# Optimization experiments

Hardware: AMD Instinct MI355X
Metric: run time of the kernel (lower is better)

The kernel has to match this reference:

```python
import jax, jax.numpy as jnp
import numpy as np


def setup_inputs() -> dict:
    key = jax.random.key(0)
    k1, k2 = jax.random.split(key)
    x = jax.random.normal(k1, (8, 2048, 512), dtype=jnp.float32)
    codebook = jax.random.normal(k2, (8192, 512), dtype=jnp.float32)
    return {"x": x, "codebook": codebook}


def reference(x, codebook):
    # x: [B, S, D]; codebook: [K, D]
    B, S, D = x.shape
    flat_x = x.reshape(-1, D)  # [N, D], N = B*S
    # argmin over L2 distance == argmin over squared L2 distance:
    x_sq = jnp.sum(flat_x * flat_x, axis=-1, keepdims=True)        # [N, 1]
    c_sq = jnp.sum(codebook * codebook, axis=-1)                   # [K]
    dots = jnp.einsum('nd,kd->nk', flat_x, codebook)               # [N, K]
    dist_sq = x_sq - 2.0 * dots + c_sq[None, :]                    # [N, K]
    indices = jnp.argmin(dist_sq, axis=1)                          # [N]
    quantized = jnp.take(codebook, indices, axis=0)                # [N, D]
    return quantized.reshape(x.shape)
```

## Files before the change

### kernel.cpp

```cpp
#include <hip/hip_runtime.h>
#include <cstdint>

constexpr int DD = 512;
constexpr int KK = 8192;
constexpr int NROWS = 16384;
#define MARGIN 1.0f

constexpr size_t AX_ELEMS = (size_t)NROWS * DD;
constexpr size_t BF_ELEMS = (size_t)KK * DD;
constexpr size_t KEY_ELEMS = (size_t)NROWS * 128;
constexpr size_t WS_NEEDED =
    AX_ELEMS * 2 + BF_ELEMS * 2 + (size_t)KK * 4 + KEY_ELEMS * 8;

typedef __attribute__((ext_vector_type(8))) short short8v;
typedef __attribute__((ext_vector_type(8))) _Float16 half8v;
typedef __attribute__((ext_vector_type(4))) float floatx4;
typedef unsigned long long ull;

__device__ __forceinline__ ull umin64(ull a, ull b) { return a < b ? a : b; }
__device__ __forceinline__ uint32_t fsort(float f) {
  uint32_t u = __float_as_uint(f);
  return (u & 0x80000000u) ? ~u : (u | 0x80000000u);
}
__device__ __forceinline__ float funsort(uint32_t u) {
  uint32_t f = (u & 0x80000000u) ? (u ^ 0x80000000u) : ~u;
  return __uint_as_float(f);
}

__device__ __forceinline__ void gl_lds16(const ushort* g, ushort* l) {
  __builtin_amdgcn_global_load_lds(
      (const __attribute__((address_space(1))) unsigned int*)g,
      (__attribute__((address_space(3))) unsigned int*)l, 16, 0, 0);
}

__device__ __forceinline__ float pairwise128_sq(const float* __restrict__ p) {
#pragma clang fp contract(off)
  float r[8];
  {
    float4 a = ((const float4*)p)[0];
    float4 b = ((const float4*)p)[1];
    r[0] = a.x * a.x; r[1] = a.y * a.y; r[2] = a.z * a.z; r[3] = a.w * a.w;
    r[4] = b.x * b.x; r[5] = b.y * b.y; r[6] = b.z * b.z; r[7] = b.w * b.w;
  }
  for (int i = 2; i < 32; i += 2) {
    float4 a = ((const float4*)p)[i];
    float4 b = ((const float4*)p)[i + 1];
    r[0] = r[0] + a.x * a.x; r[1] = r[1] + a.y * a.y;
    r[2] = r[2] + a.z * a.z; r[3] = r[3] + a.w * a.w;
    r[4] = r[4] + b.x * b.x; r[5] = r[5] + b.y * b.y;
    r[6] = r[6] + b.z * b.z; r[7] = r[7] + b.w * b.w;
  }
  return ((r[0] + r[1]) + (r[2] + r[3])) + ((r[4] + r[5]) + (r[6] + r[7]));
}

__global__ __launch_bounds__(256)
void cast16_kernel(const float* __restrict__ src, ushort* __restrict__ dst) {
  int idx = blockIdx.x * 256 + threadIdx.x;
  float4 v = *(const float4*)(src + (size_t)idx * 4);
  ushort h[4];
  float vv[4] = {v.x, v.y, v.z, v.w};
#pragma unroll
  for (int i = 0; i < 4; ++i) h[i] = __builtin_bit_cast(ushort, (_Float16)vv[i]);
  *(ushort4*)(dst + (size_t)idx * 4) = make_ushort4(h[0], h[1], h[2], h[3]);
}

__global__ __launch_bounds__(256)
void csq_kernel(const float* __restrict__ CB, float* __restrict__ csq) {
  __shared__ float cblk[64][4];
  int t = threadIdx.x;
  int r0 = blockIdx.x * 64;
  int row = t >> 2, blk = t & 3;
  cblk[row][blk] = pairwise128_sq(CB + (size_t)(r0 + row) * DD + blk * 128);
  __syncthreads();
  if (t < 64) {
#pragma clang fp contract(off)
    csq[r0 + t] = (cblk[t][0] + cblk[t][1]) + (cblk[t][2] + cblk[t][3]);
  }
}

__global__ __launch_bounds__(256, 4)
void vq_screen16_kernel(const ushort* __restrict__ Axp, const ushort* __restrict__ Bfp,
                        const float* __restrict__ csq, ull* __restrict__ keys) {
  __shared__ ushort AS[128 * 64];
  __shared__ ushort BS[128 * 64];
  __shared__ ull mb[128][2][2];

  const int t = threadIdx.x;
  const int L = t & 63;
  const int w = t >> 6;
  const int wr = (w >> 1) * 64, wc = (w & 1) * 64;

  const int bid = blockIdx.x;
  const int swz = (bid & 7) * 1024 + (bid >> 3);
  const int rb = swz & 127, cb = swz >> 7;
  const size_t r0 = (size_t)rb * 128, c0 = (size_t)cb * 128;

  const int lrow = L >> 3;
  const int lgr = (L & 7) ^ lrow;
  const ushort* srcA0 = Axp + (r0 + w * 32 + lrow) * DD + lgr * 8;
  const ushort* srcB0 = Bfp + (c0 + w * 32 + lrow) * DD + lgr * 8;

  floatx4 acc[4][4];
#pragma unroll
  for (int m = 0; m < 4; ++m)
#pragma unroll
    for (int n = 0; n < 4; ++n) acc[m][n] = (floatx4){0.f, 0.f, 0.f, 0.f};

  for (int kc = 0; kc < 8; ++kc) {
    if (kc) __syncthreads();
#pragma unroll
    for (int j = 0; j < 4; ++j) {
      gl_lds16(srcA0 + (size_t)j * 8 * DD + kc * 64, &AS[(w * 32 + j * 8) * 64]);
      gl_lds16(srcB0 + (size_t)j * 8 * DD + kc * 64, &BS[(w * 32 + j * 8) * 64]);
    }
    __syncthreads();

#pragma unroll
    for (int s = 0; s < 2; ++s) {
      const int kcol = s * 4 + (L >> 4);
      half8v af[4], bf[4];
#pragma unroll
      for (int m = 0; m < 4; ++m) {
        const int rl = wr + m * 16 + (L & 15);
        af[m] = *(const half8v*)&AS[rl * 64 + ((kcol * 8) ^ ((rl & 7) * 8))];
      }
#pragma unroll
      for (int n = 0; n < 4; ++n) {
        const int cl = wc + n * 16 + (L & 15);
        bf[n] = *(const half8v*)&BS[cl * 64 + ((kcol * 8) ^ ((cl & 7) * 8))];
      }
#pragma unroll
      for (int m = 0; m < 4; ++m)
#pragma unroll
        for (int n = 0; n < 4; ++n)
          acc[m][n] = __builtin_amdgcn_mfma_f32_16x16x32_f16(af[m], bf[n], acc[m][n], 0, 0, 0);
    }
  }

  float cq[4];
#pragma unroll
  for (int n = 0; n < 4; ++n) cq[n] = csq[c0 + wc + n * 16 + (L & 15)];

#pragma unroll
  for (int m = 0; m < 4; ++m) {
#pragma unroll
    for (int i = 0; i < 4; ++i) {
      ull k1 = ~0ull, k2 = ~0ull;
#pragma unroll
      for (int n = 0; n < 4; ++n) {
        float q = cq[n] - 2.0f * acc[m][n][i];
        ull key = ((ull)fsort(q) << 32) | (uint32_t)(c0 + wc + n * 16 + (L & 15));
        if (key < k1) { k2 = k1; k1 = key; }
        else if (key < k2) k2 = key;
      }
#pragma unroll
      for (int mask = 1; mask <= 8; mask <<= 1) {
        ull o1 = __shfl_xor(k1, mask, 64);
        ull o2 = __shfl_xor(k2, mask, 64);
        if (o1 < k1) { ull n2 = umin64(k1, o2); k1 = o1; k2 = n2; }
        else { k2 = umin64(o1, k2); }
      }
      if ((L & 15) == 0) {
        int rl = wr + m * 16 + (L >> 4) * 4 + i;
        mb[rl][w & 1][0] = k1;
        mb[rl][w & 1][1] = k2;
      }
    }
  }
  __syncthreads();
  if (t < 128) {
    ull a1 = mb[t][0][0], a2 = mb[t][0][1];
    ull b1 = mb[t][1][0], b2 = mb[t][1][1];
    ull k1, k2;
    if (a1 < b1) { k1 = a1; k2 = umin64(a2, b1); }
    else { k1 = b1; k2 = umin64(b2, a1); }
    keys[(r0 + t) * 128 + cb * 2 + 0] = k1;
    keys[(r0 + t) * 128 + cb * 2 + 1] = k2;
  }
}

__global__ __launch_bounds__(256)
void vq_reduce_kernel(const float* __restrict__ X, const float* __restrict__ CB,
                      const float* __restrict__ csq, const ull* __restrict__ keys,
                      float* __restrict__ out) {
  __shared__ int bidx[4];
  const int t = threadIdx.x;
  const int L = t & 63;
  const int w = t >> 6;
  const size_t row = (size_t)blockIdx.x * 4 + w;
  ulonglong2 kk = *(const ulonglong2*)(keys + row * 128 + L * 2);

  ull kmin = umin64(kk.x, kk.y);
#pragma unroll
  for (int m = 32; m; m >>= 1) {
    ull o = __shfl_xor(kmin, m, 64);
    if (o < kmin) kmin = o;
  }
  const float qcut = funsort((uint32_t)(kmin >> 32)) + MARGIN;

  const bool q0 = funsort((uint32_t)(kk.x >> 32)) <= qcut;
  const bool q1 = funsort((uint32_t)(kk.y >> 32)) <= qcut;
  const ull b0 = __ballot(q0);
  const ull b1 = __ballot(q1);
  const int total = __popcll(b0) + __popcll(b1);

  int winner;
  if (total <= 1) {
    winner = (int)(kmin & 0xffffffffu);
  } else {
    const float* xp = X + row * DD;
    const float4 xa = ((const float4*)xp)[L * 2];
    const float4 xb = ((const float4*)xp)[L * 2 + 1];
    ull bestE = ~0ull;
#pragma unroll
    for (int pass = 0; pass < 2; ++pass) {
      ull mask = pass ? b1 : b0;
      while (mask) {
        const int lane = __ffsll(mask) - 1;
        mask &= mask - 1;
        const ull key = __shfl(pass ? kk.y : kk.x, lane, 64);
        const int idx = (int)(key & 0xffffffffu);
        const float* cp = CB + (size_t)idx * DD;
        const float4 ca = ((const float4*)cp)[L * 2];
        const float4 cbv = ((const float4*)cp)[L * 2 + 1];
        float p = 0.f;
        p = __builtin_fmaf(xa.x, ca.x, p);
        p = __builtin_fmaf(xa.y, ca.y, p);
        p = __builtin_fmaf(xa.z, ca.z, p);
        p = __builtin_fmaf(xa.w, ca.w, p);
        p = __builtin_fmaf(xb.x, cbv.x, p);
        p = __builtin_fmaf(xb.y, cbv.y, p);
        p = __builtin_fmaf(xb.z, cbv.z, p);
        p = __builtin_fmaf(xb.w, cbv.w, p);
#pragma unroll
        for (int m = 32; m; m >>= 1) p += __shfl_xor(p, m, 64);
        const float q = csq[idx] - 2.0f * p;
        const ull ek = ((ull)fsort(q) << 32) | (uint32_t)idx;
        bestE = umin64(bestE, ek);
      }
    }
    winner = (int)(bestE & 0xffffffffu);
  }
  if (L == 0) bidx[w] = winner;
  __syncthreads();

  const size_t r0 = (size_t)blockIdx.x * 4;
#pragma unroll
  for (int it = 0; it < 2; ++it) {
    int idx = t + it * 256;
    int rw = idx >> 7, c4 = idx & 127;
    float4 v = *(const float4*)(CB + (size_t)bidx[rw] * DD + c4 * 4);
    *(float4*)(out + (r0 + rw) * DD + c4 * 4) = v;
  }
}

constexpr int FBM = 128, FBN = 128, FBK = 32, FNT = 256;
constexpr int FKSPLIT = 4;
constexpr int FKPB = KK / FKSPLIT;

__global__ __launch_bounds__(FNT)
void vq_partial_kernel(const float* __restrict__ X, const float* __restrict__ CB,
                       float* __restrict__ keyout) {
  __shared__ float Xs[FBK][FBM + 4];
  __shared__ float Cs[FBK][FBN + 4];
  __shared__ float xblk[FBM][4];
  __shared__ float cblk[FBN][4];
  __shared__ float xsq[FBM];
  __shared__ float csq[FBN];

  const int t = threadIdx.x;
  const int tx = t & 15;
  const int ty = t >> 4;
  const int bid = blockIdx.x;
  const int xcd = bid & 7;
  const int loc = bid >> 3;
  const int ksplit = xcd >> 1;
  const int rowblk = (xcd & 1) * 64 + loc;
  const long r0 = (long)rowblk * FBM;
  const int kbase = ksplit * FKPB;

#pragma unroll
  for (int it = 0; it < 2; ++it) {
    int task = t + it * FNT;
    int row = task >> 2, blk = task & 3;
    xblk[row][blk] = pairwise128_sq(X + (r0 + row) * DD + blk * 128);
  }
  __syncthreads();
  if (t < FBM) {
#pragma clang fp contract(off)
    xsq[t] = (xblk[t][0] + xblk[t][1]) + (xblk[t][2] + xblk[t][3]);
  }

  uint64_t bestKey[8];
#pragma unroll
  for (int i = 0; i < 8; ++i) bestKey[i] = ~0ull;

  float4 xr[4], cr[4];
  for (int kt = 0; kt < FKPB / FBN; ++kt) {
    const int k0 = kbase + kt * FBN;
    __syncthreads();
#pragma unroll
    for (int it = 0; it < 4; ++it) {
      int idx = t + it * FNT;
      int row = idx >> 3, dg = (idx & 7) * 4;
      xr[it] = *(const float4*)(X + (r0 + row) * DD + dg);
      cr[it] = *(const float4*)(CB + (long)(k0 + row) * DD + dg);
    }
#pragma unroll
    for (int it = 0; it < 2; ++it) {
      int task = t + it * FNT;
      int cw = task >> 2, blk = task & 3;
      cblk[cw][blk] = pairwise128_sq(CB + (long)(k0 + cw) * DD + blk * 128);
    }
    __syncthreads();
    if (t < FBN) {
#pragma clang fp contract(off)
      csq[t] = (cblk[t][0] + cblk[t][1]) + (cblk[t][2] + cblk[t][3]);
    }

    float acc[8][8];
#pragma unroll
    for (int i = 0; i < 8; ++i)
#pragma unroll
      for (int j = 0; j < 8; ++j) acc[i][j] = 0.0f;

    for (int dc = 0; dc < DD; dc += FBK) {
#pragma unroll
      for (int it = 0; it < 4; ++it) {
        int idx = t + it * FNT;
        int row = idx >> 3, dg = (idx & 7) * 4;
        Xs[dg + 0][row] = xr[it].x; Xs[dg + 1][row] = xr[it].y;
        Xs[dg + 2][row] = xr[it].z; Xs[dg + 3][row] = xr[it].w;
        Cs[dg + 0][row] = cr[it].x; Cs[dg + 1][row] = cr[it].y;
        Cs[dg + 2][row] = cr[it].z; Cs[dg + 3][row] = cr[it].w;
      }
      if (dc + FBK < DD) {
#pragma unroll
        for (int it = 0; it < 4; ++it) {
          int idx = t + it * FNT;
          int row = idx >> 3, dg = (idx & 7) * 4 + dc + FBK;
          xr[it] = *(const float4*)(X + (r0 + row) * DD + dg);
          cr[it] = *(const float4*)(CB + (long)(k0 + row) * DD + dg);
        }
      }
      __syncthreads();
#pragma unroll 4
      for (int d = 0; d < FBK; ++d) {
        const float4 xa0 = *(const float4*)&Xs[d][ty * 4];
        const float4 xa1 = *(const float4*)&Xs[d][64 + ty * 4];
        const float4 cb0 = *(const float4*)&Cs[d][tx * 4];
        const float4 cb1 = *(const float4*)&Cs[d][64 + tx * 4];
        const float xv[8] = {xa0.x, xa0.y, xa0.z, xa0.w, xa1.x, xa1.y, xa1.z, xa1.w};
        const float cv[8] = {cb0.x, cb0.y, cb0.z, cb0.w, cb1.x, cb1.y, cb1.z, cb1.w};
#pragma unroll
        for (int i = 0; i < 8; ++i)
#pragma unroll
          for (int j = 0; j < 8; ++j)
            acc[i][j] = __builtin_fmaf(xv[i], cv[j], acc[i][j]);
      }
      __syncthreads();
    }
    {
#pragma clang fp contract(off)
#pragma unroll
      for (int i = 0; i < 8; ++i) {
        int rl = (i < 4) ? (ty * 4 + i) : (64 + ty * 4 + (i - 4));
        float xsv = xsq[rl];
#pragma unroll
        for (int j = 0; j < 8; ++j) {
          int cl = (j < 4) ? (tx * 4 + j) : (64 + tx * 4 + (j - 4));
          float m = 2.0f * acc[i][j];
          float t1 = xsv - m;
          float dist = t1 + csq[cl];
          uint64_t key = ((uint64_t)fsort(dist) << 32) | (uint32_t)(k0 + cl);
          if (key < bestKey[i]) bestKey[i] = key;
        }
      }
    }
  }
#pragma unroll
  for (int i = 0; i < 8; ++i) {
    ull k = bestKey[i];
#pragma unroll
    for (int m = 1; m <= 8; m <<= 1) {
      ull o = __shfl_xor(k, m, 64);
      if (o < k) k = o;
    }
    if (tx == 0) {
      int rl = (i < 4) ? (ty * 4 + i) : (64 + ty * 4 + (i - 4));
      *(ull*)(keyout + (r0 + rl) * DD + ksplit * 2) = k;
    }
  }
}

__global__ __launch_bounds__(FNT)
void vq_reduce_gather_kernel(const float* __restrict__ CB, float* __restrict__ out) {
  __shared__ int bidx[32];
  const int t = threadIdx.x;
  const long r0 = (long)blockIdx.x * 32;
  if (t < 32) {
    const ull* kp = (const ull*)(out + (r0 + t) * DD);
    ull k = kp[0];
#pragma unroll
    for (int s = 1; s < FKSPLIT; ++s) k = umin64(k, kp[s]);
    bidx[t] = (int)(k & 0xffffffffu);
  }
  __syncthreads();
#pragma unroll
  for (int it = 0; it < 16; ++it) {
    int idx = t + it * FNT;
    int row = idx >> 7, c4 = idx & 127;
    const float4 v = *(const float4*)(CB + (long)bidx[row] * DD + c4 * 4);
    *(float4*)(out + (r0 + row) * DD + c4 * 4) = v;
  }
}

extern "C" void kernel_launch(void* const* d_in, const int* in_sizes, int n_in,
                              void* d_out, int out_size, void* d_ws, size_t ws_size,
                              hipStream_t stream) {
  const float* X = (const float*)d_in[0];
  const float* CB = (const float*)d_in[1];
  float* out = (float*)d_out;

  if (ws_size >= WS_NEEDED) {
    ushort* Axp = (ushort*)d_ws;
    ushort* Bfp = Axp + AX_ELEMS;
    float* csqp = (float*)(Bfp + BF_ELEMS);
    ull* keys = (ull*)(csqp + KK);
    hipLaunchKernelGGL(cast16_kernel, dim3(NROWS * DD / 4 / 256), dim3(256), 0, stream, X, Axp);
    hipLaunchKernelGGL(cast16_kernel, dim3(KK * DD / 4 / 256), dim3(256), 0, stream, CB, Bfp);
    hipLaunchKernelGGL(csq_kernel, dim3(KK / 64), dim3(256), 0, stream, CB, csqp);
    hipLaunchKernelGGL(vq_screen16_kernel, dim3((NROWS / 128) * (KK / 128)), dim3(256), 0, stream,
                       Axp, Bfp, csqp, keys);
    hipLaunchKernelGGL(vq_reduce_kernel, dim3(NROWS / 4), dim3(256), 0, stream,
                       X, CB, csqp, keys, out);
  } else {
    hipLaunchKernelGGL(vq_partial_kernel, dim3(512), dim3(FNT), 0, stream, X, CB, out);
    hipLaunchKernelGGL(vq_reduce_gather_kernel, dim3(NROWS / 32), dim3(FNT), 0, stream, CB, out);
  }
}
```

Measured before the change: 265.9 us.

## Enlarge screening GEMM tile to 256x256 with double-buffered LDS staging

The fp16 MFMA screening kernel moves from 128x128 tiles with 256 threads to 256x256 tiles with 512 threads (8 waves, each computing 128x64), and double-buffers the A/B LDS stages so the next K-slice load overlaps the current MFMAs. The larger tile halves the global operand traffic per output and halves the number of candidate keys written per row, so the reduce kernel reads one key per lane. The trade-off is more LDS (two 64 KB buffers) and 128 accumulator registers per thread, which limits occupancy and may cause register spills. There are also fewer blocks (2048) to spread across the CUs.

```diff
diff --git a/kernel.cpp b/kernel.cpp
--- a/kernel.cpp
+++ b/kernel.cpp
@@ -8,7 +8,7 @@
 
 constexpr size_t AX_ELEMS = (size_t)NROWS * DD;
 constexpr size_t BF_ELEMS = (size_t)KK * DD;
-constexpr size_t KEY_ELEMS = (size_t)NROWS * 128;
+constexpr size_t KEY_ELEMS = (size_t)NROWS * 64;
 constexpr size_t WS_NEEDED =
     AX_ELEMS * 2 + BF_ELEMS * 2 + (size_t)KK * 4 + KEY_ELEMS * 8;
 
@@ -78,78 +78,90 @@
   }
 }
 
-__global__ __launch_bounds__(256, 4)
-void vq_screen16_kernel(const ushort* __restrict__ Axp, const ushort* __restrict__ Bfp,
-                        const float* __restrict__ csq, ull* __restrict__ keys) {
-  __shared__ ushort AS[128 * 64];
-  __shared__ ushort BS[128 * 64];
-  __shared__ ull mb[128][2][2];
+__global__ __launch_bounds__(512, 2)
+void vq_screen256_kernel(const ushort* __restrict__ Axp, const ushort* __restrict__ Bfp,
+                         const float* __restrict__ csq, ull* __restrict__ keys) {
+  __shared__ ushort AS[2][256 * 64];
+  __shared__ ushort BS[2][256 * 64];
+  __shared__ ull mb[256][4][2];
 
   const int t = threadIdx.x;
   const int L = t & 63;
   const int w = t >> 6;
-  const int wr = (w >> 1) * 64, wc = (w & 1) * 64;
+  const int wr = w >> 2;
+  const int wc = w & 3;
 
   const int bid = blockIdx.x;
-  const int swz = (bid & 7) * 1024 + (bid >> 3);
-  const int rb = swz & 127, cb = swz >> 7;
-  const size_t r0 = (size_t)rb * 128, c0 = (size_t)cb * 128;
+  const int swz = (bid & 7) * 256 + (bid >> 3);
+  const int rb = swz & 63, cb = swz >> 6;
+  const size_t r0 = (size_t)rb * 256, c0 = (size_t)cb * 256;
 
   const int lrow = L >> 3;
   const int lgr = (L & 7) ^ lrow;
   const ushort* srcA0 = Axp + (r0 + w * 32 + lrow) * DD + lgr * 8;
   const ushort* srcB0 = Bfp + (c0 + w * 32 + lrow) * DD + lgr * 8;
 
-  floatx4 acc[4][4];
-#pragma unroll
-  for (int m = 0; m < 4; ++m)
+  floatx4 acc[8][4];
+#pragma unroll
+  for (int m = 0; m < 8; ++m)
 #pragma unroll
     for (int n = 0; n < 4; ++n) acc[m][n] = (floatx4){0.f, 0.f, 0.f, 0.f};
 
-  for (int kc = 0; kc < 8; ++kc) {
-    if (kc) __syncthreads();
-#pragma unroll
-    for (int j = 0; j < 4; ++j) {
-      gl_lds16(srcA0 + (size_t)j * 8 * DD + kc * 64, &AS[(w * 32 + j * 8) * 64]);
-      gl_lds16(srcB0 + (size_t)j * 8 * DD + kc * 64, &BS[(w * 32 + j * 8) * 64]);
-    }
-    __syncthreads();
-
-#pragma unroll
-    for (int s = 0; s < 2; ++s) {
-      const int kcol = s * 4 + (L >> 4);
-      half8v af[4], bf[4];
-#pragma unroll
-      for (int m = 0; m < 4; ++m) {
-        const int rl = wr + m * 16 + (L & 15);
-        af[m] = *(const half8v*)&AS[rl * 64 + ((kcol * 8) ^ ((rl & 7) * 8))];
+#define STAGE(KS, BUF)                                                          \
+  {                                                                             \
+    _Pragma("unroll") for (int j = 0; j < 4; ++j) {                             \
+      gl_lds16(srcA0 + (size_t)j * 8 * DD + (KS) * 64,                          \
+               &AS[BUF][(w * 32 + j * 8) * 64]);                                \
+      gl_lds16(srcB0 + (size_t)j * 8 * DD + (KS) * 64,                          \
+               &BS[BUF][(w * 32 + j * 8) * 64]);                                \
+    }                                                                           \
+  }
+
+  STAGE(0, 0);
+  __syncthreads();
+
+  int buf = 0;
+  for (int ks = 0; ks < 8; ++ks) {
+    if (ks < 7) STAGE(ks + 1, buf ^ 1);
+
+#pragma unroll
+    for (int kc = 0; kc < 2; ++kc) {
+      const int kcol = kc * 4 + (L >> 4);
+      half8v af[8], bf[4];
+#pragma unroll
+      for (int m = 0; m < 8; ++m) {
+        const int rl = wr * 128 + m * 16 + (L & 15);
+        af[m] = *(const half8v*)&AS[buf][rl * 64 + ((kcol * 8) ^ ((rl & 7) * 8))];
       }
 #pragma unroll
       for (int n = 0; n < 4; ++n) {
-        const int cl = wc + n * 16 + (L & 15);
-        bf[n] = *(const half8v*)&BS[cl * 64 + ((kcol * 8) ^ ((cl & 7) * 8))];
-      }
-#pragma unroll
-      for (int m = 0; m < 4; ++m)
+        const int cl = wc * 64 + n * 16 + (L & 15);
+        bf[n] = *(const half8v*)&BS[buf][cl * 64 + ((kcol * 8) ^ ((cl & 7) * 8))];
+      }
+#pragma unroll
+      for (int m = 0; m < 8; ++m)
 #pragma unroll
         for (int n = 0; n < 4; ++n)
           acc[m][n] = __builtin_amdgcn_mfma_f32_16x16x32_f16(af[m], bf[n], acc[m][n], 0, 0, 0);
     }
-  }
+    __syncthreads();
+    buf ^= 1;
+  }
+#undef STAGE
 
   float cq[4];
 #pragma unroll
-  for (int n = 0; n < 4; ++n) cq[n] = csq[c0 + wc + n * 16 + (L & 15)];
-
-#pragma unroll
-  for (int m = 0; m < 4; ++m) {
+  for (int n = 0; n < 4; ++n) cq[n] = csq[c0 + wc * 64 + n * 16 + (L & 15)];
+
+#pragma unroll
+  for (int m = 0; m < 8; ++m) {
 #pragma unroll
     for (int i = 0; i < 4; ++i) {
       ull k1 = ~0ull, k2 = ~0ull;
 #pragma unroll
       for (int n = 0; n < 4; ++n) {
         float q = cq[n] - 2.0f * acc[m][n][i];
-        ull key = ((ull)fsort(q) << 32) | (uint32_t)(c0 + wc + n * 16 + (L & 15));
+        ull key = ((ull)fsort(q) << 32) | (uint32_t)(c0 + wc * 64 + n * 16 + (L & 15));
         if (key < k1) { k2 = k1; k1 = key; }
         else if (key < k2) k2 = key;
       }
@@ -161,21 +173,24 @@
         else { k2 = umin64(o1, k2); }
       }
       if ((L & 15) == 0) {
-        int rl = wr + m * 16 + (L >> 4) * 4 + i;
-        mb[rl][w & 1][0] = k1;
-        mb[rl][w & 1][1] = k2;
-      }
-    }
-  }
-  __syncthreads();
-  if (t < 128) {
-    ull a1 = mb[t][0][0], a2 = mb[t][0][1];
-    ull b1 = mb[t][1][0], b2 = mb[t][1][1];
-    ull k1, k2;
-    if (a1 < b1) { k1 = a1; k2 = umin64(a2, b1); }
-    else { k1 = b1; k2 = umin64(b2, a1); }
-    keys[(r0 + t) * 128 + cb * 2 + 0] = k1;
-    keys[(r0 + t) * 128 + cb * 2 + 1] = k2;
+        int rl = wr * 128 + m * 16 + (L >> 4) * 4 + i;
+        mb[rl][wc][0] = k1;
+        mb[rl][wc][1] = k2;
+      }
+    }
+  }
+  __syncthreads();
+
+  if (t < 256) {
+    ull k1 = ~0ull, k2 = ~0ull;
+#pragma unroll
+    for (int s = 0; s < 4; ++s) {
+      ull a1 = mb[t][s][0], a2 = mb[t][s][1];
+      if (a1 < k1) { k2 = umin64(k1, a2); k1 = a1; }
+      else { k2 = umin64(k2, a1); }
+    }
+    keys[(r0 + t) * 64 + cb * 2 + 0] = k1;
+    keys[(r0 + t) * 64 + cb * 2 + 1] = k2;
   }
 }
 
@@ -188,9 +203,9 @@
   const int L = t & 63;
   const int w = t >> 6;
   const size_t row = (size_t)blockIdx.x * 4 + w;
-  ulonglong2 kk = *(const ulonglong2*)(keys + row * 128 + L * 2);
-
-  ull kmin = umin64(kk.x, kk.y);
+  const ull kx = keys[row * 64 + L];
+
+  ull kmin = kx;
 #pragma unroll
   for (int m = 32; m; m >>= 1) {
     ull o = __shfl_xor(kmin, m, 64);
@@ -198,11 +213,9 @@
   }
   const float qcut = funsort((uint32_t)(kmin >> 32)) + MARGIN;
 
-  const bool q0 = funsort((uint32_t)(kk.x >> 32)) <= qcut;
-  const bool q1 = funsort((uint32_t)(kk.y >> 32)) <= qcut;
-  const ull b0 = __ballot(q0);
-  const ull b1 = __ballot(q1);
-  const int total = __popcll(b0) + __popcll(b1);
+  const bool qc = funsort((uint32_t)(kx >> 32)) <= qcut;
+  const ull b = __ballot(qc);
+  const int total = __popcll(b);
 
   int winner;
   if (total <= 1) {
@@ -212,32 +225,29 @@
     const float4 xa = ((const float4*)xp)[L * 2];
     const float4 xb = ((const float4*)xp)[L * 2 + 1];
     ull bestE = ~0ull;
-#pragma unroll
-    for (int pass = 0; pass < 2; ++pass) {
-      ull mask = pass ? b1 : b0;
-      while (mask) {
-        const int lane = __ffsll(mask) - 1;
-        mask &= mask - 1;
-        const ull key = __shfl(pass ? kk.y : kk.x, lane, 64);
-        const int idx = (int)(key & 0xffffffffu);
-        const float* cp = CB + (size_t)idx * DD;
-        const float4 ca = ((const float4*)cp)[L * 2];
-        const float4 cbv = ((const float4*)cp)[L * 2 + 1];
-        float p = 0.f;
-        p = __builtin_fmaf(xa.x, ca.x, p);
-        p = __builtin_fmaf(xa.y, ca.y, p);
-        p = __builtin_fmaf(xa.z, ca.z, p);
-        p = __builtin_fmaf(xa.w, ca.w, p);
-        p = __builtin_fmaf(xb.x, cbv.x, p);
-        p = __builtin_fmaf(xb.y, cbv.y, p);
-        p = __builtin_fmaf(xb.z, cbv.z, p);
-        p = __builtin_fmaf(xb.w, cbv.w, p);
-#pragma unroll
-        for (int m = 32; m; m >>= 1) p += __shfl_xor(p, m, 64);
-        const float q = csq[idx] - 2.0f * p;
-        const ull ek = ((ull)fsort(q) << 32) | (uint32_t)idx;
-        bestE = umin64(bestE, ek);
-      }
+    ull mask = b;
+    while (mask) {
+      const int lane = __ffsll(mask) - 1;
+      mask &= mask - 1;
+      const ull key = __shfl(kx, lane, 64);
+      const int idx = (int)(key & 0xffffffffu);
+      const float* cp = CB + (size_t)idx * DD;
+      const float4 ca = ((const float4*)cp)[L * 2];
+      const float4 cbv = ((const float4*)cp)[L * 2 + 1];
+      float p = 0.f;
+      p = __builtin_fmaf(xa.x, ca.x, p);
+      p = __builtin_fmaf(xa.y, ca.y, p);
+      p = __builtin_fmaf(xa.z, ca.z, p);
+      p = __builtin_fmaf(xa.w, ca.w, p);
+      p = __builtin_fmaf(xb.x, cbv.x, p);
+      p = __builtin_fmaf(xb.y, cbv.y, p);
+      p = __builtin_fmaf(xb.z, cbv.z, p);
+      p = __builtin_fmaf(xb.w, cbv.w, p);
+#pragma unroll
+      for (int m = 32; m; m >>= 1) p += __shfl_xor(p, m, 64);
+      const float q = csq[idx] - 2.0f * p;
+      const ull ek = ((ull)fsort(q) << 32) | (uint32_t)idx;
+      bestE = umin64(bestE, ek);
     }
     winner = (int)(bestE & 0xffffffffu);
   }
@@ -430,8 +440,8 @@
     hipLaunchKernelGGL(cast16_kernel, dim3(NROWS * DD / 4 / 256), dim3(256), 0, stream, X, Axp);
     hipLaunchKernelGGL(cast16_kernel, dim3(KK * DD / 4 / 256), dim3(256), 0, stream, CB, Bfp);
     hipLaunchKernelGGL(csq_kernel, dim3(KK / 64), dim3(256), 0, stream, CB, csqp);
-    hipLaunchKernelGGL(vq_screen16_kernel, dim3((NROWS / 128) * (KK / 128)), dim3(256), 0, stream,
-                       Axp, Bfp, csqp, keys);
+    hipLaunchKernelGGL(vq_screen256_kernel, dim3((NROWS / 256) * (KK / 256)), dim3(512), 0,
+                       stream, Axp, Bfp, csqp, keys);
     hipLaunchKernelGGL(vq_reduce_kernel, dim3(NROWS / 4), dim3(256), 0, stream,
                        X, CB, csqp, keys, out);
   } else {
```

New measurement: 296.3 us. 11.4% more time.
